# Optimization experiments

Measured on AMD Instinct MI355X. Metric: run time of the kernel, lower is better.

Reference implementation:

```python
import jax, jax.numpy as jnp
import numpy as np

CR = 32  # channels // reduction

def setup_inputs() -> dict:
    key = jax.random.key(0)
    k1, k2 = jax.random.split(key)
    x = jax.random.normal(k1, (1, 64, 8, 32, 32), dtype=jnp.float32)
    W = jax.random.normal(k2, (CR, 64), dtype=jnp.float32) * (1.0 / np.sqrt(64.0))
    bias = jnp.zeros((CR,), dtype=jnp.float32)
    return {"x": x, "W": W, "bias": bias}

def reference(x, W, bias):
    b, c, d, h, w = x.shape
    cr = W.shape[0]
    n = d * h * w
    # 1x1x1 Conv3d == per-voxel linear projection over channels
    x_red = jnp.einsum('oc,bcdhw->bodhw', W, x) + bias[None, :, None, None, None]
    q = x_red.reshape(b, cr, n)          # [b, cr, N]
    k = q                                 # shared projection (q == k)
    v = x.reshape(b, c, n)               # [b, c, N]
    # attn[b, i, j] = <q[:, i], k[:, j]>, softmax over j (dim=2)
    attn = jnp.einsum('bci,bcj->bij', q, k) / jnp.sqrt(jnp.float32(cr))
    attn = jax.nn.softmax(attn, axis=2)
    # out[b, c, m] = sum_n v[b, c, n] * attn[b, n, m]  (torch.bmm(v, attn))
    out = jnp.einsum('bcn,bnm->bcm', v, attn)
    out = out.reshape(b, c, d, h, w)
    return out + x
```

## Files before the change

kernel.cpp:

```cpp
#include <hip/hip_runtime.h>

#define N_TOK 8192

typedef _Float16 f16x8 __attribute__((ext_vector_type(8)));
typedef _Float16 f16x4 __attribute__((ext_vector_type(4)));
typedef float    f32x4 __attribute__((ext_vector_type(4)));

__device__ __forceinline__ f32x4 mfma_k32(f16x8 a, f16x8 b, f32x4 c) {
  return __builtin_amdgcn_mfma_f32_16x16x32_f16(a, b, c, 0, 0, 0);
}
__device__ __forceinline__ f32x4 mfma_k16(f16x4 a, f16x4 b, f32x4 c) {
  return __builtin_amdgcn_mfma_f32_16x16x16f16(a, b, c, 0, 0, 0);
}

#define QSCALE 0.50500977f

__global__ __launch_bounds__(1024) void prep_kernel(
    const float* __restrict__ x, const float* __restrict__ W,
    const float* __restrict__ bias, _Float16* __restrict__ qe,
    _Float16* __restrict__ vht, float* __restrict__ Ln,
    float* __restrict__ out) {
  __shared__ float Wl[32 * 65];
  __shared__ float xl[64 * 36];
  int t = threadIdx.x, b = blockIdx.x;
  int n0 = b * 32;
  if (b < 8) Ln[b * 1024 + t] = 0.f;
  for (int i = t; i < 2048; i += 1024) Wl[(i >> 6) * 65 + (i & 63)] = W[i];
  if (t < 512) {
    int c = t >> 3, j4 = t & 7;
    f32x4 v = *(const f32x4*)(x + c * N_TOK + n0 + j4 * 4);
    *(f32x4*)&xl[c * 36 + j4 * 4] = v;
    *(f32x4*)(out + c * N_TOK + n0 + j4 * 4) = v;
    f16x4 hv;
#pragma unroll
    for (int j = 0; j < 4; ++j) hv[j] = (_Float16)v[j];
    int q = j4 & 3, h = j4 >> 2;
    *(f16x4*)(vht + b * 2048 + c * 32 + q * 8 + h * 4) = hv;
  }
  __syncthreads();
  int nl = t >> 5, o = t & 31;
  float a0 = bias[o], a1 = 0.f;
#pragma unroll
  for (int c = 0; c < 32; ++c) {
    a0 = fmaf(Wl[o * 65 + c], xl[c * 36 + nl], a0);
    a1 = fmaf(Wl[o * 65 + 32 + c], xl[(32 + c) * 36 + nl], a1);
  }
  qe[(n0 + nl) * 32 + o] = (_Float16)((a0 + a1) * QSCALE);
}

__global__ __launch_bounds__(1024) void pass1_kernel(
    const _Float16* __restrict__ qe, float* __restrict__ Ln) {
  __shared__ float Lp[16][64];
  int t = threadIdx.x, b = blockIdx.x;
  int w = t >> 6, lane = t & 63, quad = lane >> 4, l15 = lane & 15;
  int n0 = (b >> 1) * 64;
  int mbase = (b & 1) * 4096 + w * 256;
  f16x8 af[4];
#pragma unroll
  for (int g = 0; g < 4; ++g)
    af[g] = *(const f16x8*)(qe + (n0 + g * 16 + l15) * 32 + quad * 8);
  f32x4 sums[4];
#pragma unroll
  for (int g = 0; g < 4; ++g) sums[g] = f32x4{0.f, 0.f, 0.f, 0.f};
  for (int mt = 0; mt < 8; ++mt) {
    int m0 = mbase + mt * 32;
    f16x8 bf0 = *(const f16x8*)(qe + (m0 + l15) * 32 + quad * 8);
    f16x8 bf1 = *(const f16x8*)(qe + (m0 + 16 + l15) * 32 + quad * 8);
    f32x4 zero = {0.f, 0.f, 0.f, 0.f};
#pragma unroll
    for (int g = 0; g < 4; ++g) {
      f32x4 s0 = mfma_k32(af[g], bf0, zero);
      f32x4 s1 = mfma_k32(af[g], bf1, zero);
#pragma unroll
      for (int r = 0; r < 4; ++r)
        sums[g][r] +=
            __builtin_amdgcn_exp2f(s0[r]) + __builtin_amdgcn_exp2f(s1[r]);
    }
  }
#pragma unroll
  for (int g = 0; g < 4; ++g)
#pragma unroll
    for (int r = 0; r < 4; ++r)
#pragma unroll
      for (int mask = 1; mask < 16; mask <<= 1)
        sums[g][r] += __shfl_xor(sums[g][r], mask, 64);
  if (l15 == 0) {
#pragma unroll
    for (int g = 0; g < 4; ++g)
      *(f32x4*)&Lp[w][g * 16 + quad * 4] = sums[g];
  }
  __syncthreads();
  if (t < 64) {
    float L = 0.f;
#pragma unroll
    for (int ww = 0; ww < 16; ++ww) L += Lp[ww][t];
    unsafeAtomicAdd(Ln + n0 + t, L);
  }
}

__global__ __launch_bounds__(1024, 4) void pass2_kernel(
    const _Float16* __restrict__ qe, const _Float16* __restrict__ vht,
    const float* __restrict__ Ln, float* __restrict__ out) {
  __shared__ float Ot[4 * 64 * 65];
  int t = threadIdx.x, b = blockIdx.x;
  int w = t >> 6, lane = t & 63, quad = lane >> 4, l15 = lane & 15;
  int m0 = (b >> 1) * 64;
  int nh = b & 1;
  int chalf = w >> 3, nseg = w & 7;
  int nbase = nh * 4096 + nseg * 512;

  f16x8 bm[4];
#pragma unroll
  for (int mt = 0; mt < 4; ++mt)
    bm[mt] = *(const f16x8*)(qe + (m0 + mt * 16 + l15) * 32 + quad * 8);

  f32x4 acc[2][4];
#pragma unroll
  for (int ct = 0; ct < 2; ++ct)
#pragma unroll
    for (int mt = 0; mt < 4; ++mt) acc[ct][mt] = f32x4{0.f, 0.f, 0.f, 0.f};

  for (int ch = 0; ch < 16; ++ch) {
    int nb = nbase + ch * 32;
    f16x8 an0 = *(const f16x8*)(qe + (nb + l15) * 32 + quad * 8);
    f16x8 an1 = *(const f16x8*)(qe + (nb + 16 + l15) * 32 + quad * 8);
    f32x4 Lq0 = *(const f32x4*)(Ln + nb + quad * 4);
    f32x4 Lq1 = *(const f32x4*)(Ln + nb + 16 + quad * 4);
    const _Float16* vb =
        vht + (nb >> 5) * 2048 + (chalf * 32) * 32 + l15 * 32 + quad * 8;
    f16x8 av0 = *(const f16x8*)(vb);
    f16x8 av1 = *(const f16x8*)(vb + 512);
    f32x4 Bq0, Bq1;
#pragma unroll
    for (int r = 0; r < 4; ++r) {
      Bq0[r] = __builtin_amdgcn_logf(Lq0[r]);
      Bq1[r] = __builtin_amdgcn_logf(Lq1[r]);
    }
    f32x4 zero = {0.f, 0.f, 0.f, 0.f};
    f16x4 p0[4], p1[4];
#pragma unroll
    for (int mt = 0; mt < 4; ++mt) {
      f32x4 s0 = mfma_k32(an0, bm[mt], zero);
      f32x4 s1 = mfma_k32(an1, bm[mt], zero);
#pragma unroll
      for (int r = 0; r < 4; ++r) {
        p0[mt][r] = (_Float16)__builtin_amdgcn_exp2f(s0[r] - Bq0[r]);
        p1[mt][r] = (_Float16)__builtin_amdgcn_exp2f(s1[r] - Bq1[r]);
      }
    }
#pragma unroll
    for (int ct = 0; ct < 2; ++ct) {
      f16x8 av = (ct == 0) ? av0 : av1;
      f16x4 lo, hi;
#pragma unroll
      for (int j = 0; j < 4; ++j) {
        lo[j] = av[j];
        hi[j] = av[j + 4];
      }
#pragma unroll
      for (int mt = 0; mt < 4; ++mt) {
        acc[ct][mt] = mfma_k16(lo, p0[mt], acc[ct][mt]);
        acc[ct][mt] = mfma_k16(hi, p1[mt], acc[ct][mt]);
      }
    }
  }

  if (nseg < 4) {
#pragma unroll
    for (int ct = 0; ct < 2; ++ct)
#pragma unroll
      for (int mt = 0; mt < 4; ++mt)
#pragma unroll
        for (int r = 0; r < 4; ++r)
          Ot[(nseg * 64 + chalf * 32 + ct * 16 + quad * 4 + r) * 65 +
             mt * 16 + l15] = acc[ct][mt][r];
  }
  __syncthreads();
  if (nseg >= 4) {
#pragma unroll
    for (int ct = 0; ct < 2; ++ct)
#pragma unroll
      for (int mt = 0; mt < 4; ++mt)
#pragma unroll
        for (int r = 0; r < 4; ++r)
          Ot[((nseg - 4) * 64 + chalf * 32 + ct * 16 + quad * 4 + r) * 65 +
             mt * 16 + l15] += acc[ct][mt][r];
  }
  __syncthreads();
  for (int idx = t; idx < 4096; idx += 1024) {
    int cc = idx >> 6, m = idx & 63;
    float v = 0.f;
#pragma unroll
    for (int s = 0; s < 4; ++s) v += Ot[(s * 64 + cc) * 65 + m];
    unsafeAtomicAdd(out + cc * N_TOK + m0 + m, v);
  }
}

extern "C" void kernel_launch(void* const* d_in, const int* in_sizes, int n_in,
                              void* d_out, int out_size, void* d_ws,
                              size_t ws_size, hipStream_t stream) {
  const float* x = (const float*)d_in[0];
  const float* W = (const float*)d_in[1];
  const float* bias = (const float*)d_in[2];
  float* out = (float*)d_out;

  char* ws = (char*)d_ws;
  _Float16* qe = (_Float16*)ws;
  _Float16* vht = (_Float16*)(ws + 524288);
  float* Ln = (float*)(ws + 524288 + 1048576);

  prep_kernel<<<256, 1024, 0, stream>>>(x, W, bias, qe, vht, Ln, out);
  pass1_kernel<<<256, 1024, 0, stream>>>(qe, Ln);
  pass2_kernel<<<256, 1024, 0, stream>>>(qe, vht, Ln, out);
}
```

Measured before the change: 99.85 us.

## Fuse softmax-denominator and output passes into one kernel with grid barrier

Merges pass1 and pass2 into a single persistent kernel. A global atomic counter acts as a grid-wide barrier between computing the row sums Ln and computing the output. The log of Ln is precomputed once per block into shared memory and fed in as the MFMA accumulator init, so the subtraction in the inner loop goes away. This removes one kernel launch and the per-chunk log work. In exchange it relies on all 256 blocks being co-resident, and the spin-wait adds barrier latency.

```diff
diff --git a/kernel.cpp b/kernel.cpp
--- a/kernel.cpp
+++ b/kernel.cpp
@@ -19,12 +19,13 @@
     const float* __restrict__ x, const float* __restrict__ W,
     const float* __restrict__ bias, _Float16* __restrict__ qe,
     _Float16* __restrict__ vht, float* __restrict__ Ln,
-    float* __restrict__ out) {
+    int* __restrict__ cnt, float* __restrict__ out) {
   __shared__ float Wl[32 * 65];
   __shared__ float xl[64 * 36];
   int t = threadIdx.x, b = blockIdx.x;
   int n0 = b * 32;
   if (b < 8) Ln[b * 1024 + t] = 0.f;
+  if (b == 8 && t == 0) *cnt = 0;
   for (int i = t; i < 2048; i += 1024) Wl[(i >> 6) * 65 + (i & 63)] = W[i];
   if (t < 512) {
     int c = t >> 3, j4 = t & 7;
@@ -48,151 +49,169 @@
   qe[(n0 + nl) * 32 + o] = (_Float16)((a0 + a1) * QSCALE);
 }
 
-__global__ __launch_bounds__(1024) void pass1_kernel(
-    const _Float16* __restrict__ qe, float* __restrict__ Ln) {
-  __shared__ float Lp[16][64];
+__global__ __launch_bounds__(1024, 4) void mega_kernel(
+    const _Float16* __restrict__ qe, const _Float16* __restrict__ vht,
+    float* __restrict__ Ln, int* __restrict__ cnt, float* __restrict__ out) {
+  __shared__ union {
+    float Lp[16][64];
+    struct {
+      float Bl[4096];
+      float Ot[4 * 64 * 65];
+    } p2;
+  } sm;
   int t = threadIdx.x, b = blockIdx.x;
   int w = t >> 6, lane = t & 63, quad = lane >> 4, l15 = lane & 15;
-  int n0 = (b >> 1) * 64;
-  int mbase = (b & 1) * 4096 + w * 256;
-  f16x8 af[4];
-#pragma unroll
-  for (int g = 0; g < 4; ++g)
-    af[g] = *(const f16x8*)(qe + (n0 + g * 16 + l15) * 32 + quad * 8);
-  f32x4 sums[4];
-#pragma unroll
-  for (int g = 0; g < 4; ++g) sums[g] = f32x4{0.f, 0.f, 0.f, 0.f};
-  for (int mt = 0; mt < 8; ++mt) {
-    int m0 = mbase + mt * 32;
-    f16x8 bf0 = *(const f16x8*)(qe + (m0 + l15) * 32 + quad * 8);
-    f16x8 bf1 = *(const f16x8*)(qe + (m0 + 16 + l15) * 32 + quad * 8);
-    f32x4 zero = {0.f, 0.f, 0.f, 0.f};
-#pragma unroll
-    for (int g = 0; g < 4; ++g) {
-      f32x4 s0 = mfma_k32(af[g], bf0, zero);
-      f32x4 s1 = mfma_k32(af[g], bf1, zero);
+  int rt = b >> 1, half = b & 1;
+
+  {
+    int n0 = rt * 64;
+    int mbase = half * 4096 + w * 256;
+    f16x8 af[4];
+#pragma unroll
+    for (int g = 0; g < 4; ++g)
+      af[g] = *(const f16x8*)(qe + (n0 + g * 16 + l15) * 32 + quad * 8);
+    f32x4 sums[4];
+#pragma unroll
+    for (int g = 0; g < 4; ++g) sums[g] = f32x4{0.f, 0.f, 0.f, 0.f};
+    for (int mt = 0; mt < 8; ++mt) {
+      int m0 = mbase + mt * 32;
+      f16x8 bf0 = *(const f16x8*)(qe + (m0 + l15) * 32 + quad * 8);
+      f16x8 bf1 = *(const f16x8*)(qe + (m0 + 16 + l15) * 32 + quad * 8);
+      f32x4 zero = {0.f, 0.f, 0.f, 0.f};
+#pragma unroll
+      for (int g = 0; g < 4; ++g) {
+        f32x4 s0 = mfma_k32(af[g], bf0, zero);
+        f32x4 s1 = mfma_k32(af[g], bf1, zero);
+#pragma unroll
+        for (int r = 0; r < 4; ++r)
+          sums[g][r] +=
+              __builtin_amdgcn_exp2f(s0[r]) + __builtin_amdgcn_exp2f(s1[r]);
+      }
+    }
+#pragma unroll
+    for (int g = 0; g < 4; ++g)
 #pragma unroll
       for (int r = 0; r < 4; ++r)
-        sums[g][r] +=
-            __builtin_amdgcn_exp2f(s0[r]) + __builtin_amdgcn_exp2f(s1[r]);
-    }
-  }
-#pragma unroll
-  for (int g = 0; g < 4; ++g)
-#pragma unroll
-    for (int r = 0; r < 4; ++r)
-#pragma unroll
-      for (int mask = 1; mask < 16; mask <<= 1)
-        sums[g][r] += __shfl_xor(sums[g][r], mask, 64);
-  if (l15 == 0) {
-#pragma unroll
-    for (int g = 0; g < 4; ++g)
-      *(f32x4*)&Lp[w][g * 16 + quad * 4] = sums[g];
-  }
-  __syncthreads();
-  if (t < 64) {
-    float L = 0.f;
-#pragma unroll
-    for (int ww = 0; ww < 16; ++ww) L += Lp[ww][t];
-    unsafeAtomicAdd(Ln + n0 + t, L);
-  }
-}
-
-__global__ __launch_bounds__(1024, 4) void pass2_kernel(
-    const _Float16* __restrict__ qe, const _Float16* __restrict__ vht,
-    const float* __restrict__ Ln, float* __restrict__ out) {
-  __shared__ float Ot[4 * 64 * 65];
-  int t = threadIdx.x, b = blockIdx.x;
-  int w = t >> 6, lane = t & 63, quad = lane >> 4, l15 = lane & 15;
-  int m0 = (b >> 1) * 64;
-  int nh = b & 1;
-  int chalf = w >> 3, nseg = w & 7;
-  int nbase = nh * 4096 + nseg * 512;
-
-  f16x8 bm[4];
-#pragma unroll
-  for (int mt = 0; mt < 4; ++mt)
-    bm[mt] = *(const f16x8*)(qe + (m0 + mt * 16 + l15) * 32 + quad * 8);
-
-  f32x4 acc[2][4];
-#pragma unroll
-  for (int ct = 0; ct < 2; ++ct)
-#pragma unroll
-    for (int mt = 0; mt < 4; ++mt) acc[ct][mt] = f32x4{0.f, 0.f, 0.f, 0.f};
-
-  for (int ch = 0; ch < 16; ++ch) {
-    int nb = nbase + ch * 32;
-    f16x8 an0 = *(const f16x8*)(qe + (nb + l15) * 32 + quad * 8);
-    f16x8 an1 = *(const f16x8*)(qe + (nb + 16 + l15) * 32 + quad * 8);
-    f32x4 Lq0 = *(const f32x4*)(Ln + nb + quad * 4);
-    f32x4 Lq1 = *(const f32x4*)(Ln + nb + 16 + quad * 4);
-    const _Float16* vb =
-        vht + (nb >> 5) * 2048 + (chalf * 32) * 32 + l15 * 32 + quad * 8;
-    f16x8 av0 = *(const f16x8*)(vb);
-    f16x8 av1 = *(const f16x8*)(vb + 512);
-    f32x4 Bq0, Bq1;
-#pragma unroll
-    for (int r = 0; r < 4; ++r) {
-      Bq0[r] = __builtin_amdgcn_logf(Lq0[r]);
-      Bq1[r] = __builtin_amdgcn_logf(Lq1[r]);
-    }
-    f32x4 zero = {0.f, 0.f, 0.f, 0.f};
-    f16x4 p0[4], p1[4];
-#pragma unroll
-    for (int mt = 0; mt < 4; ++mt) {
-      f32x4 s0 = mfma_k32(an0, bm[mt], zero);
-      f32x4 s1 = mfma_k32(an1, bm[mt], zero);
-#pragma unroll
-      for (int r = 0; r < 4; ++r) {
-        p0[mt][r] = (_Float16)__builtin_amdgcn_exp2f(s0[r] - Bq0[r]);
-        p1[mt][r] = (_Float16)__builtin_amdgcn_exp2f(s1[r] - Bq1[r]);
+#pragma unroll
+        for (int mask = 1; mask < 16; mask <<= 1)
+          sums[g][r] += __shfl_xor(sums[g][r], mask, 64);
+    if (l15 == 0) {
+#pragma unroll
+      for (int g = 0; g < 4; ++g)
+        *(f32x4*)&sm.Lp[w][g * 16 + quad * 4] = sums[g];
+    }
+    __syncthreads();
+    if (t < 64) {
+      float L = 0.f;
+#pragma unroll
+      for (int ww = 0; ww < 16; ++ww) L += sm.Lp[ww][t];
+      unsafeAtomicAdd(Ln + n0 + t, L);
+    }
+  }
+
+  __threadfence();
+  __syncthreads();
+  if (t == 0) {
+    __hip_atomic_fetch_add(cnt, 1, __ATOMIC_ACQ_REL, __HIP_MEMORY_SCOPE_AGENT);
+    while (__hip_atomic_load(cnt, __ATOMIC_ACQUIRE,
+                             __HIP_MEMORY_SCOPE_AGENT) < 256)
+      __builtin_amdgcn_s_sleep(2);
+  }
+  __syncthreads();
+
+  for (int i = t; i < 4096; i += 1024) {
+    float L = __hip_atomic_load(Ln + half * 4096 + i, __ATOMIC_RELAXED,
+                                __HIP_MEMORY_SCOPE_AGENT);
+    sm.p2.Bl[i] = -__builtin_amdgcn_logf(L);
+  }
+  __syncthreads();
+
+  {
+    int m0 = rt * 64;
+    int chalf = w >> 3, nseg = w & 7;
+    int nbl0 = nseg * 512;
+    int nhb = half * 4096;
+
+    f16x8 bm[4];
+#pragma unroll
+    for (int mt = 0; mt < 4; ++mt)
+      bm[mt] = *(const f16x8*)(qe + (m0 + mt * 16 + l15) * 32 + quad * 8);
+
+    f32x4 acc[2][4];
+#pragma unroll
+    for (int ct = 0; ct < 2; ++ct)
+#pragma unroll
+      for (int mt = 0; mt < 4; ++mt) acc[ct][mt] = f32x4{0.f, 0.f, 0.f, 0.f};
+
+    for (int ch = 0; ch < 16; ++ch) {
+      int nbl = nbl0 + ch * 32;
+      int nb = nhb + nbl;
+      f16x8 an0 = *(const f16x8*)(qe + (nb + l15) * 32 + quad * 8);
+      f16x8 an1 = *(const f16x8*)(qe + (nb + 16 + l15) * 32 + quad * 8);
+      f32x4 nBq0 = *(const f32x4*)&sm.p2.Bl[nbl + quad * 4];
+      f32x4 nBq1 = *(const f32x4*)&sm.p2.Bl[nbl + 16 + quad * 4];
+      const _Float16* vb =
+          vht + (nb >> 5) * 2048 + chalf * 1024 + l15 * 32 + quad * 8;
+      f16x8 av0 = *(const f16x8*)(vb);
+      f16x8 av1 = *(const f16x8*)(vb + 512);
+      f16x4 p0[4], p1[4];
+#pragma unroll
+      for (int mt = 0; mt < 4; ++mt) {
+        f32x4 s0 = mfma_k32(an0, bm[mt], nBq0);
+        f32x4 s1 = mfma_k32(an1, bm[mt], nBq1);
+#pragma unroll
+        for (int r = 0; r < 4; ++r) {
+          p0[mt][r] = (_Float16)__builtin_amdgcn_exp2f(s0[r]);
+          p1[mt][r] = (_Float16)__builtin_amdgcn_exp2f(s1[r]);
+        }
       }
-    }
-#pragma unroll
-    for (int ct = 0; ct < 2; ++ct) {
-      f16x8 av = (ct == 0) ? av0 : av1;
-      f16x4 lo, hi;
-#pragma unroll
-      for (int j = 0; j < 4; ++j) {
-        lo[j] = av[j];
-        hi[j] = av[j + 4];
+#pragma unroll
+      for (int ct = 0; ct < 2; ++ct) {
+        f16x8 av = (ct == 0) ? av0 : av1;
+        f16x4 lo, hi;
+#pragma unroll
+        for (int j = 0; j < 4; ++j) {
+          lo[j] = av[j];
+          hi[j] = av[j + 4];
+        }
+#pragma unroll
+        for (int mt = 0; mt < 4; ++mt) {
+          acc[ct][mt] = mfma_k16(lo, p0[mt], acc[ct][mt]);
+          acc[ct][mt] = mfma_k16(hi, p1[mt], acc[ct][mt]);
+        }
       }
-#pragma unroll
-      for (int mt = 0; mt < 4; ++mt) {
-        acc[ct][mt] = mfma_k16(lo, p0[mt], acc[ct][mt]);
-        acc[ct][mt] = mfma_k16(hi, p1[mt], acc[ct][mt]);
-      }
-    }
-  }
-
-  if (nseg < 4) {
-#pragma unroll
-    for (int ct = 0; ct < 2; ++ct)
-#pragma unroll
-      for (int mt = 0; mt < 4; ++mt)
-#pragma unroll
-        for (int r = 0; r < 4; ++r)
-          Ot[(nseg * 64 + chalf * 32 + ct * 16 + quad * 4 + r) * 65 +
-             mt * 16 + l15] = acc[ct][mt][r];
-  }
-  __syncthreads();
-  if (nseg >= 4) {
-#pragma unroll
-    for (int ct = 0; ct < 2; ++ct)
-#pragma unroll
-      for (int mt = 0; mt < 4; ++mt)
-#pragma unroll
-        for (int r = 0; r < 4; ++r)
-          Ot[((nseg - 4) * 64 + chalf * 32 + ct * 16 + quad * 4 + r) * 65 +
-             mt * 16 + l15] += acc[ct][mt][r];
-  }
-  __syncthreads();
-  for (int idx = t; idx < 4096; idx += 1024) {
-    int cc = idx >> 6, m = idx & 63;
-    float v = 0.f;
-#pragma unroll
-    for (int s = 0; s < 4; ++s) v += Ot[(s * 64 + cc) * 65 + m];
-    unsafeAtomicAdd(out + cc * N_TOK + m0 + m, v);
+    }
+
+    __syncthreads();
+    if (nseg < 4) {
+#pragma unroll
+      for (int ct = 0; ct < 2; ++ct)
+#pragma unroll
+        for (int mt = 0; mt < 4; ++mt)
+#pragma unroll
+          for (int r = 0; r < 4; ++r)
+            sm.p2.Ot[(nseg * 64 + chalf * 32 + ct * 16 + quad * 4 + r) * 65 +
+                     mt * 16 + l15] = acc[ct][mt][r];
+    }
+    __syncthreads();
+    if (nseg >= 4) {
+#pragma unroll
+      for (int ct = 0; ct < 2; ++ct)
+#pragma unroll
+        for (int mt = 0; mt < 4; ++mt)
+#pragma unroll
+          for (int r = 0; r < 4; ++r)
+            sm.p2.Ot[((nseg - 4) * 64 + chalf * 32 + ct * 16 + quad * 4 + r) *
+                         65 + mt * 16 + l15] += acc[ct][mt][r];
+    }
+    __syncthreads();
+    for (int idx = t; idx < 4096; idx += 1024) {
+      int cc = idx >> 6, m = idx & 63;
+      float v = 0.f;
+#pragma unroll
+      for (int s = 0; s < 4; ++s) v += sm.p2.Ot[(s * 64 + cc) * 65 + m];
+      unsafeAtomicAdd(out + cc * N_TOK + m0 + m, v);
+    }
   }
 }
 
@@ -207,9 +226,9 @@
   char* ws = (char*)d_ws;
   _Float16* qe = (_Float16*)ws;
   _Float16* vht = (_Float16*)(ws + 524288);
-  float* Ln = (float*)(ws + 524288 + 1048576);
-
-  prep_kernel<<<256, 1024, 0, stream>>>(x, W, bias, qe, vht, Ln, out);
-  pass1_kernel<<<256, 1024, 0, stream>>>(qe, Ln);
-  pass2_kernel<<<256, 1024, 0, stream>>>(qe, vht, Ln, out);
-}
+  float* Ln = (float*)(ws + 1572864);
+  int* cnt = (int*)(ws + 1605632);
+
+  prep_kernel<<<256, 1024, 0, stream>>>(x, W, bias, qe, vht, Ln, cnt, out);
+  mega_kernel<<<256, 1024, 0, stream>>>(qe, vht, Ln, cnt, out);
+}
```

New measurement: 161.7 us. 61.9% more time.

## Repartition pass2 warps over m-halves and fold log-normalizer into MFMA accumulator

Applied to the files above, without the earlier changes.

Pass2 warps now split work by n-segment and m-half instead of channel-half and n-segment. Each warp computes the exp scores for 32 query columns and applies them to all 64 channels, so each exponential is computed once and reused across all four channel tiles instead of being recomputed per channel half. The per-token negative log normalizers are computed once per block into shared memory and passed as the MFMA accumulator init, which removes the per-iteration log and subtract. The cost is an extra shared buffer and sync, plus four V fragment loads per iteration instead of two.

```diff
diff --git a/kernel.cpp b/kernel.cpp
--- a/kernel.cpp
+++ b/kernel.cpp
@@ -101,89 +101,87 @@
 __global__ __launch_bounds__(1024, 4) void pass2_kernel(
     const _Float16* __restrict__ qe, const _Float16* __restrict__ vht,
     const float* __restrict__ Ln, float* __restrict__ out) {
+  __shared__ float Bl[4096];
   __shared__ float Ot[4 * 64 * 65];
   int t = threadIdx.x, b = blockIdx.x;
   int w = t >> 6, lane = t & 63, quad = lane >> 4, l15 = lane & 15;
   int m0 = (b >> 1) * 64;
-  int nh = b & 1;
-  int chalf = w >> 3, nseg = w & 7;
-  int nbase = nh * 4096 + nseg * 512;
-
-  f16x8 bm[4];
-#pragma unroll
-  for (int mt = 0; mt < 4; ++mt)
-    bm[mt] = *(const f16x8*)(qe + (m0 + mt * 16 + l15) * 32 + quad * 8);
-
-  f32x4 acc[2][4];
-#pragma unroll
-  for (int ct = 0; ct < 2; ++ct)
-#pragma unroll
-    for (int mt = 0; mt < 4; ++mt) acc[ct][mt] = f32x4{0.f, 0.f, 0.f, 0.f};
+  int half = b & 1;
+  int nseg = w >> 1, mhalf = w & 1;
+  int nhb = half * 4096, nbl0 = nseg * 512;
+
+  for (int i = t; i < 4096; i += 1024)
+    Bl[i] = -__builtin_amdgcn_logf(Ln[nhb + i]);
+  __syncthreads();
+
+  f16x8 bm[2];
+#pragma unroll
+  for (int mt = 0; mt < 2; ++mt)
+    bm[mt] =
+        *(const f16x8*)(qe + (m0 + mhalf * 32 + mt * 16 + l15) * 32 + quad * 8);
+
+  f32x4 acc[4][2];
+#pragma unroll
+  for (int ct = 0; ct < 4; ++ct)
+#pragma unroll
+    for (int mt = 0; mt < 2; ++mt) acc[ct][mt] = f32x4{0.f, 0.f, 0.f, 0.f};
 
   for (int ch = 0; ch < 16; ++ch) {
-    int nb = nbase + ch * 32;
+    int nbl = nbl0 + ch * 32;
+    int nb = nhb + nbl;
     f16x8 an0 = *(const f16x8*)(qe + (nb + l15) * 32 + quad * 8);
     f16x8 an1 = *(const f16x8*)(qe + (nb + 16 + l15) * 32 + quad * 8);
-    f32x4 Lq0 = *(const f32x4*)(Ln + nb + quad * 4);
-    f32x4 Lq1 = *(const f32x4*)(Ln + nb + 16 + quad * 4);
-    const _Float16* vb =
-        vht + (nb >> 5) * 2048 + (chalf * 32) * 32 + l15 * 32 + quad * 8;
-    f16x8 av0 = *(const f16x8*)(vb);
-    f16x8 av1 = *(const f16x8*)(vb + 512);
-    f32x4 Bq0, Bq1;
-#pragma unroll
-    for (int r = 0; r < 4; ++r) {
-      Bq0[r] = __builtin_amdgcn_logf(Lq0[r]);
-      Bq1[r] = __builtin_amdgcn_logf(Lq1[r]);
-    }
-    f32x4 zero = {0.f, 0.f, 0.f, 0.f};
-    f16x4 p0[4], p1[4];
-#pragma unroll
-    for (int mt = 0; mt < 4; ++mt) {
-      f32x4 s0 = mfma_k32(an0, bm[mt], zero);
-      f32x4 s1 = mfma_k32(an1, bm[mt], zero);
+    f32x4 nBq0 = *(const f32x4*)&Bl[nbl + quad * 4];
+    f32x4 nBq1 = *(const f32x4*)&Bl[nbl + 16 + quad * 4];
+    const _Float16* vb = vht + (nb >> 5) * 2048 + l15 * 32 + quad * 8;
+    f16x8 av[4];
+#pragma unroll
+    for (int ct = 0; ct < 4; ++ct)
+      av[ct] = *(const f16x8*)(vb + ct * 512);
+#pragma unroll
+    for (int mt = 0; mt < 2; ++mt) {
+      f32x4 s0 = mfma_k32(an0, bm[mt], nBq0);
+      f32x4 s1 = mfma_k32(an1, bm[mt], nBq1);
+      f16x4 p0, p1;
 #pragma unroll
       for (int r = 0; r < 4; ++r) {
-        p0[mt][r] = (_Float16)__builtin_amdgcn_exp2f(s0[r] - Bq0[r]);
-        p1[mt][r] = (_Float16)__builtin_amdgcn_exp2f(s1[r] - Bq1[r]);
+        p0[r] = (_Float16)__builtin_amdgcn_exp2f(s0[r]);
+        p1[r] = (_Float16)__builtin_amdgcn_exp2f(s1[r]);
+      }
+#pragma unroll
+      for (int ct = 0; ct < 4; ++ct) {
+        f16x4 lo, hi;
+#pragma unroll
+        for (int j = 0; j < 4; ++j) {
+          lo[j] = av[ct][j];
+          hi[j] = av[ct][j + 4];
+        }
+        acc[ct][mt] = mfma_k16(lo, p0, acc[ct][mt]);
+        acc[ct][mt] = mfma_k16(hi, p1, acc[ct][mt]);
       }
     }
-#pragma unroll
-    for (int ct = 0; ct < 2; ++ct) {
-      f16x8 av = (ct == 0) ? av0 : av1;
-      f16x4 lo, hi;
-#pragma unroll
-      for (int j = 0; j < 4; ++j) {
-        lo[j] = av[j];
-        hi[j] = av[j + 4];
-      }
-#pragma unroll
-      for (int mt = 0; mt < 4; ++mt) {
-        acc[ct][mt] = mfma_k16(lo, p0[mt], acc[ct][mt]);
-        acc[ct][mt] = mfma_k16(hi, p1[mt], acc[ct][mt]);
-      }
-    }
-  }
-
+  }
+
+  __syncthreads();
   if (nseg < 4) {
 #pragma unroll
-    for (int ct = 0; ct < 2; ++ct)
-#pragma unroll
-      for (int mt = 0; mt < 4; ++mt)
+    for (int ct = 0; ct < 4; ++ct)
+#pragma unroll
+      for (int mt = 0; mt < 2; ++mt)
 #pragma unroll
         for (int r = 0; r < 4; ++r)
-          Ot[(nseg * 64 + chalf * 32 + ct * 16 + quad * 4 + r) * 65 +
+          Ot[(nseg * 64 + ct * 16 + quad * 4 + r) * 65 + mhalf * 32 +
              mt * 16 + l15] = acc[ct][mt][r];
   }
   __syncthreads();
   if (nseg >= 4) {
 #pragma unroll
-    for (int ct = 0; ct < 2; ++ct)
-#pragma unroll
-      for (int mt = 0; mt < 4; ++mt)
+    for (int ct = 0; ct < 4; ++ct)
+#pragma unroll
+      for (int mt = 0; mt < 2; ++mt)
 #pragma unroll
         for (int r = 0; r < 4; ++r)
-          Ot[((nseg - 4) * 64 + chalf * 32 + ct * 16 + quad * 4 + r) * 65 +
+          Ot[((nseg - 4) * 64 + ct * 16 + quad * 4 + r) * 65 + mhalf * 32 +
              mt * 16 + l15] += acc[ct][mt][r];
   }
   __syncthreads();
@@ -207,7 +205,7 @@
   char* ws = (char*)d_ws;
   _Float16* qe = (_Float16*)ws;
   _Float16* vht = (_Float16*)(ws + 524288);
-  float* Ln = (float*)(ws + 524288 + 1048576);
+  float* Ln = (float*)(ws + 1572864);
 
   prep_kernel<<<256, 1024, 0, stream>>>(x, W, bias, qe, vht, Ln, out);
   pass1_kernel<<<256, 1024, 0, stream>>>(qe, Ln);
```

After: 99.61 us (median of 2 runs). No clear change (-0.2%).
